# Optimization experiments

Hardware: AMD Instinct MI355X
Metric: run time of the kernel (lower is better)

## Reference

```python
import jax, jax.numpy as jnp
import numpy as np

# ---- production-scale dims ----
U, I, D = 51200, 25600, 64          # users, items, embed_size
E, EP = 1_000_000, 100_000          # train edges, pos/neg scoring edges
K = 8                               # topk similar users (FFT filter length)
NF = K // 2 + 1                     # rfft bins
CL_BS = 256                         # contrastive chunk size (U % CL_BS == 0)
TEMP = 0.2                          # args.temperature
N_LAYERS = 2                        # args.layers


def setup_inputs() -> dict:
    key = jax.random.key(0)
    ks = jax.random.split(key, 14)
    return {
        "user_emb": jax.random.normal(ks[0], (U, D), jnp.float32) * 0.1,
        "item_emb": jax.random.normal(ks[1], (I, D), jnp.float32) * 0.1,
        "W": jax.random.normal(ks[2], (D, D), jnp.float32) * (1.0 / np.sqrt(D)),
        "a": jax.random.normal(ks[3], (D,), jnp.float32) * 0.1,
        "WU": jax.random.normal(ks[4], (D, D), jnp.float32) * (1.0 / np.sqrt(D)),
        "aU": jax.random.normal(ks[5], (2 * D,), jnp.float32) * 0.1,
        "complex_weight": jax.random.normal(ks[6], (1, NF, D, 2), jnp.float32) * 0.02,
        "rate_src": jax.random.randint(ks[7], (E,), 0, U),
        "rate_dst": jax.random.randint(ks[8], (E,), 0, I),
        "pos_u": jax.random.randint(ks[9], (EP,), 0, U),
        "pos_i": jax.random.randint(ks[10], (EP,), 0, I),
        "neg_u": jax.random.randint(ks[11], (EP,), 0, U),
        "neg_i": jax.random.randint(ks[12], (EP,), 0, I),
        "nbr_idx": jax.random.randint(ks[13], (U, K), 0, U),
    }


def _propagate(src_feat, src_idx, dst_idx, n_dst):
    """DGRecLayer: degree-normalized mean aggregation over bipartite edges."""
    msg = src_feat[src_idx]                                       # [E, D] gather
    agg = jax.ops.segment_sum(msg, dst_idx, num_segments=n_dst)   # [n_dst, D] scatter
    deg = jax.ops.segment_sum(jnp.ones((src_idx.shape[0],), src_feat.dtype),
                              dst_idx, num_segments=n_dst)
    return agg / jnp.maximum(deg, 1.0)[:, None]


def _layer_attention(ls, W, a):
    t = jnp.stack(ls, axis=0)                                     # [L+1, N, D]
    alpha = jax.nn.softmax(jnp.einsum('lnd,de,e->ln', t, W, a), axis=0)
    return jnp.einsum('lnd,ln->nd', t, alpha)


def _anchor_user_embed(user_emb, WU, aU, complex_weight, nbr_idx):
    # Original detaches user embeddings to numpy for the FAISS path.
    ue = jax.lax.stop_gradient(user_emb)
    simu = ue[nbr_idx]                                            # [U, K, D]
    x = jnp.fft.rfft(simu, axis=1, norm='ortho')                  # [U, NF, D]
    wc = complex_weight[..., 0] + 1j * complex_weight[..., 1]     # [1, NF, D]
    simu = jnp.fft.irfft(x * wc, n=K, axis=1, norm='ortho')       # [U, K, D]
    Wsimu = jnp.einsum('ukd,de->uke', simu, WU)                   # [U, K, D]
    Wu = jnp.broadcast_to((ue @ WU)[:, None, :], Wsimu.shape)     # [U, K, D]
    e = jnp.concatenate([Wsimu, Wu], axis=2) @ aU                 # [U, K]
    e = jnp.where(e > 0, e, 0.1 * e)                              # LeakyReLU(0.1)
    alpha = jax.nn.softmax(e, axis=1)
    return jnp.einsum('uke,uk->ue', Wsimu, alpha)                 # [U, D]


def _chunk_contrast(r1, r2):
    B = r1.shape[0]
    n1 = jnp.linalg.norm(r1, axis=-1, keepdims=True)
    n2 = jnp.linalg.norm(r2, axis=-1, keepdims=True)
    s11 = (r1 @ r1.T) / (n1 @ n1.T + 1e-6) / TEMP
    c12 = (r1 @ r2.T) / (n1 @ n2.T + 1e-6) / TEMP
    s22 = (r2 @ r2.T) / (n2 @ n2.T + 1e-6) / TEMP
    c21 = (r2 @ r1.T) / (n2 @ n1.T + 1e-6) / TEMP
    mask = jax.nn.one_hot(jnp.arange(B), 2 * B, dtype=r1.dtype) * (-1e10)
    logits = jnp.concatenate(
        [jnp.concatenate([s11, c12], axis=-1) + mask,
         jnp.concatenate([s22, c21], axis=-1) + mask], axis=0)     # [2B, 2B]
    labels = jnp.concatenate([jnp.arange(B) + B, jnp.arange(B) + B])
    logz = jax.scipy.special.logsumexp(logits, axis=-1)
    return logz - logits[jnp.arange(2 * B), labels]                # per-example CE


def reference(user_emb, item_emb, W, a, WU, aU, complex_weight,
              rate_src, rate_dst, pos_u, pos_i, neg_u, neg_i, nbr_idx):
    h_u, h_i = user_emb, item_emb
    users, items = [h_u], [h_i]
    for _ in range(N_LAYERS):
        new_i = _propagate(h_u, rate_src, rate_dst, I)   # user -> item ('rate')
        new_u = _propagate(h_i, rate_dst, rate_src, U)   # item -> user ('rated by')
        h_u, h_i = new_u, new_i
        users.append(h_u)
        items.append(h_i)
    hu = _layer_attention(users, W, a)                   # [U, D]
    hi = _layer_attention(items, W, a)                   # [I, D]

    anchor = _anchor_user_embed(user_emb, WU, aU, complex_weight, nbr_idx)
    r1 = hu.reshape(-1, CL_BS, D)
    r2 = anchor.reshape(-1, CL_BS, D)
    loss_contrast = jax.vmap(_chunk_contrast)(r1, r2).mean()

    score_pos = jnp.sum(hu[pos_u] * hi[pos_i], axis=-1, keepdims=True)  # u_dot_v
    score_neg = jnp.sum(hu[neg_u] * hi[neg_i], axis=-1, keepdims=True)
    return score_pos, score_neg, loss_contrast
```

## Files before the change

kernel.cpp:

```cpp
#include <hip/hip_runtime.h>
#include <hip/hip_bf16.h>

constexpr int U_  = 51200;
constexpr int I_  = 25600;
constexpr int E_  = 1000000;
constexpr int EP_ = 100000;
constexpr int CB_ = 256;
constexpr int NCHUNK_ = U_ / CB_;
constexpr size_t UD_ = (size_t)U_ * 64;
constexpr size_t ID_ = (size_t)I_ * 64;
constexpr int NBK_ = 200;
constexpr int CAP_ = 8192;
constexpr int TILE_ = 4096;
constexpr int NBA_ = (E_ + TILE_ - 1) / TILE_;
constexpr int NANC_ = U_ / 16;
constexpr int NCVT_ = (int)((UD_ + ID_) / (8 * 256));

constexpr float SCALE_E_  = 16.f;
constexpr float ISCALE_E_ = 1.f / 16.f;
constexpr float SCALE_1_  = 64.f;
constexpr float ISCALE_1_ = 1.f / 64.f;

constexpr size_t OFF_LOSS  = 0;
constexpr size_t OFF_FLAG  = 1;
constexpr size_t OFF_CURU  = 8;
constexpr size_t OFF_CURI  = 208;
constexpr size_t MEMSET_BYTES = 408 * 4;
constexpr size_t OFF_VEC   = 448;
constexpr size_t OFF_BBU   = 640;
constexpr size_t OFF_BBI   = 848;
constexpr size_t OFF_ROWU  = 1088;
constexpr size_t OFF_ROWI  = ((OFF_ROWU + U_ + 1 + 63) / 64) * 64;
constexpr size_t OFF_CSRU  = ((OFF_ROWI + I_ + 1 + 63) / 64) * 64;
constexpr size_t OFF_CSRI  = OFF_CSRU + E_;
constexpr size_t OFF_U1    = ((OFF_CSRI + E_ + 63) / 64) * 64;
constexpr size_t OFF_I1    = OFF_U1 + UD_;
constexpr size_t OFF_HU    = OFF_I1 + ID_;
constexpr size_t OFF_HI    = OFF_HU + UD_;
constexpr size_t OFF_ANC   = OFF_HI + ID_;
constexpr size_t OFF_UE8   = OFF_ANC + UD_;
constexpr size_t OFF_IE8   = OFF_UE8 + UD_ / 4;
constexpr size_t OFF_U18   = OFF_IE8 + ID_ / 4;
constexpr size_t OFF_I18   = OFF_U18 + UD_ / 4;

#define DEVI static __device__ __forceinline__

typedef _Float16 h2v __attribute__((ext_vector_type(2)));
typedef _Float16 f16x8 __attribute__((ext_vector_type(8)));
typedef float floatx4 __attribute__((ext_vector_type(4)));
typedef unsigned short u16x8 __attribute__((ext_vector_type(8)));

DEVI float b2f(__hip_bfloat16 x) { return __bfloat162float(x); }

DEVI float bfb2f(unsigned short b) {
  unsigned u = ((unsigned)b) << 16; float f; __builtin_memcpy(&f, &u, 4); return f;
}

DEVI float ldf(const void* p, size_t i, int isf32) {
  if (isf32) return ((const float*)p)[i];
  return b2f(((const __hip_bfloat16*)p)[i]);
}

DEVI float frcp(float x) { return __builtin_amdgcn_rcpf(x); }

DEVI float fexp2(float x) {
#if __has_builtin(__builtin_amdgcn_exp2f)
  return __builtin_amdgcn_exp2f(x);
#else
  return exp2f(x);
#endif
}

DEVI float fp8_dec(unsigned v) {
#if __has_builtin(__builtin_amdgcn_cvt_f32_fp8)
  return __builtin_amdgcn_cvt_f32_fp8(v, 0);
#else
  unsigned b = v & 0xFF;
  if (!(b & 0x78)) return 0.f;
  unsigned short h = (unsigned short)(((b & 0x80) << 8) | (((b & 0x7f) + (8 << 3)) << 7));
  _Float16 hf; __builtin_memcpy(&hf, &h, 2);
  return (float)hf;
#endif
}

#if __has_builtin(__builtin_amdgcn_cvt_f32_fp8)
#define FP8D(w, s) __builtin_amdgcn_cvt_f32_fp8((w), (s))
#else
#define FP8D(w, s) fp8_dec(((w) >> (8 * (s))) & 0xFF)
#endif

DEVI unsigned fp8_enc_pk(float a, float b) {
#if __has_builtin(__builtin_amdgcn_cvt_pk_fp8_f32)
  return __builtin_amdgcn_cvt_pk_fp8_f32(a, b, 0u, false);
#else
  auto enc1 = [](float f) -> unsigned {
    _Float16 hf = (_Float16)f; unsigned short hb; __builtin_memcpy(&hb, &hf, 2);
    int s = hb >> 15, e = (hb >> 10) & 31, m = hb & 1023;
    int e8 = e - 15 + 7;
    int m3 = (m + ((1 << 6) + ((m >> 7) & 1))) >> 7;
    if (m3 > 7) { m3 = 0; e8++; }
    if (e8 <= 0) return (unsigned)(s << 7);
    if (e8 > 15) { e8 = 15; m3 = 6; }
    return (unsigned)((s << 7) | (e8 << 3) | m3);
  };
  return enc1(a) | (enc1(b) << 8);
#endif
}

DEVI int waveInclScan(int v, int lane) {
  #pragma unroll
  for (int off = 1; off < 64; off <<= 1) {
    int t = __shfl_up(v, off, 64);
    if (lane >= off) v += t;
  }
  return v;
}

__global__ void prep_kernel(const unsigned short* __restrict__ ueu,
                            const void* __restrict__ W, const void* __restrict__ a,
                            const void* __restrict__ WU, const void* __restrict__ aU,
                            float* __restrict__ vecs, float* __restrict__ flag) {
  int cnt = 0;
  for (int i = 0; i < 256; i++) {
    int e = (ueu[i] >> 7) & 0xFF;
    if (e >= 130) cnt++;
  }
  int isf32 = (cnt >= 8);
  if (threadIdx.x == 0) *flag = isf32 ? 1.0f : 0.0f;
  int d = threadIdx.x;
  float s = 0.f, t1 = 0.f, t2 = 0.f;
  for (int e = 0; e < 64; e++) {
    s += ldf(W, d * 64 + e, isf32) * ldf(a, e, isf32);
    float wue = ldf(WU, d * 64 + e, isf32);
    t1 += wue * ldf(aU, e, isf32);
    t2 += wue * ldf(aU, 64 + e, isf32);
  }
  vecs[d] = s;
  vecs[64 + d] = t1;
  vecs[128 + d] = t2;
}

struct BktSmem {
  int histU[NBK_], histI[NBK_];
  int loffU[NBK_ + 1], loffI[NBK_ + 1];
  int cbU[NBK_], cbI[NBK_];
  int lcU[NBK_], lcI[NBK_];
  int wsU[4], wsI[4];
  unsigned recsU[TILE_], recsI[TILE_];
};
constexpr int WS_ = 72;
struct AncSmem {
  _Float16 WUt[64 * WS_];
  _Float16 mixS[16 * WS_];
  float invSe[16];
  int nbrS[128];
};
constexpr size_t FSA_SMEM = sizeof(BktSmem) > sizeof(AncSmem) ? sizeof(BktSmem) : sizeof(AncSmem);

DEVI void bucketA_body(char* smemRaw, int blk,
    const int* __restrict__ rs, const int* __restrict__ rd,
    unsigned* __restrict__ bufU, unsigned* __restrict__ bufI,
    int* __restrict__ curU, int* __restrict__ curI) {
  BktSmem& S = *(BktSmem*)smemRaw;
  int tid = threadIdx.x;
  int base = blk * TILE_;
  for (int i = tid; i < NBK_; i += 256) { S.histU[i] = 0; S.histI[i] = 0; }
  __syncthreads();
  int ss[16], dd[16];
  #pragma unroll
  for (int t = 0; t < 16; t++) {
    int e = base + t * 256 + tid;
    bool v = e < E_;
    ss[t] = v ? rs[e] : -1;
    dd[t] = v ? rd[e] : 0;
    if (v) {
      atomicAdd(&S.histU[ss[t] >> 8], 1);
      atomicAdd(&S.histI[dd[t] >> 7], 1);
    }
  }
  __syncthreads();
  if (tid < NBK_) {
    int cU = S.histU[tid];
    S.cbU[tid] = tid * CAP_ + (cU ? atomicAdd(&curU[tid], cU) : 0);
    int cI = S.histI[tid];
    S.cbI[tid] = tid * CAP_ + (cI ? atomicAdd(&curI[tid], cI) : 0);
  }
  int lane = tid & 63, wv = tid >> 6;
  int cvU = (tid < NBK_) ? S.histU[tid] : 0;
  int cvI = (tid < NBK_) ? S.histI[tid] : 0;
  int inU = waveInclScan(cvU, lane);
  int inI = waveInclScan(cvI, lane);
  if (lane == 63) { S.wsU[wv] = inU; S.wsI[wv] = inI; }
  __syncthreads();
  int woU = 0, woI = 0;
  for (int w = 0; w < wv; w++) { woU += S.wsU[w]; woI += S.wsI[w]; }
  if (tid < NBK_) {
    S.loffU[tid] = woU + inU - cvU;
    S.loffI[tid] = woI + inI - cvI;
  }
  if (tid == NBK_ - 1) {
    S.loffU[NBK_] = woU + inU;
    S.loffI[NBK_] = woI + inI;
  }
  __syncthreads();
  if (tid < NBK_) { S.lcU[tid] = S.loffU[tid]; S.lcI[tid] = S.loffI[tid]; }
  __syncthreads();
  #pragma unroll
  for (int t = 0; t < 16; t++) {
    if (ss[t] >= 0) {
      int b = ss[t] >> 8;
      int p = atomicAdd(&S.lcU[b], 1);
      S.recsU[p] = ((unsigned)(ss[t] & 255) << 17) | (unsigned)dd[t];
      b = dd[t] >> 7;
      p = atomicAdd(&S.lcI[b], 1);
      S.recsI[p] = ((unsigned)(dd[t] & 127) << 17) | (unsigned)ss[t];
    }
  }
  __syncthreads();
  int totU = S.loffU[NBK_];
  for (int p = tid; p < totU; p += 256) {
    int lo = 0, hi = NBK_;
    while (hi - lo > 1) { int mid = (lo + hi) >> 1; if (S.loffU[mid] <= p) lo = mid; else hi = mid; }
    bufU[S.cbU[lo] + (p - S.loffU[lo])] = S.recsU[p];
  }
  int totI = S.loffI[NBK_];
  for (int p = tid; p < totI; p += 256) {
    int lo = 0, hi = NBK_;
    while (hi - lo > 1) { int mid = (lo + hi) >> 1; if (S.loffI[mid] <= p) lo = mid; else hi = mid; }
    bufI[S.cbI[lo] + (p - S.loffI[lo])] = S.recsI[p];
  }
}

DEVI void anchor_body(char* smemRaw, int blk,
    const void* __restrict__ ue, const void* __restrict__ WU,
    const void* __restrict__ cw, const float* __restrict__ vecs,
    const int* __restrict__ nbr, float* __restrict__ out, int isf32) {
  AncSmem& S = *(AncSmem*)smemRaw;
  int tid = threadIdx.x;
  int wv = tid >> 6, lane = tid & 63;
  int ublk = blk * 16;

  #pragma unroll
  for (int it = 0; it < 16; it++) {
    int k = it * 4 + wv;
    S.WUt[lane * WS_ + k] = (_Float16)ldf(WU, (size_t)k * 64 + lane, isf32);
  }
  if (tid < 128) S.nbrS[tid] = nbr[ublk * 8 + tid];
  __syncthreads();

  float cw0 = ldf(cw, (0 * 64 + lane) * 2, isf32);
  float w1r = ldf(cw, (1 * 64 + lane) * 2, isf32), w1i = ldf(cw, (1 * 64 + lane) * 2 + 1, isf32);
  float w2r = ldf(cw, (2 * 64 + lane) * 2, isf32), w2i = ldf(cw, (2 * 64 + lane) * 2 + 1, isf32);
  float w3r = ldf(cw, (3 * 64 + lane) * 2, isf32), w3i = ldf(cw, (3 * 64 + lane) * 2 + 1, isf32);
  float cw4 = ldf(cw, (4 * 64 + lane) * 2, isf32);
  float v1 = vecs[64 + lane], v2 = vecs[128 + lane];
  const float c1 = 0.70710678118654752440f;

  float xc[8], xn[8];
  #pragma unroll
  for (int k = 0; k < 8; k++)
    xc[k] = ldf(ue, (size_t)S.nbrS[wv * 32 + k] * 64 + lane, isf32);

  for (int u4 = 0; u4 < 4; u4++) {
    int uL = wv * 4 + u4;
    int u = ublk + uL;
    if (u4 < 3) {
      #pragma unroll
      for (int k = 0; k < 8; k++)
        xn[k] = ldf(ue, (size_t)S.nbrS[wv * 32 + (u4 + 1) * 8 + k] * 64 + lane, isf32);
    }
    float sA = xc[1] - xc[3] - xc[5] + xc[7];
    float sB = xc[1] + xc[3] - xc[5] - xc[7];
    float ev = (xc[0] + xc[4]) + (xc[2] + xc[6]);
    float od = (xc[1] + xc[5]) + (xc[3] + xc[7]);
    float d04 = xc[0] - xc[4], d26 = xc[2] - xc[6];
    float X0r = ev + od;
    float X1r = d04 + c1 * sA;
    float X1i = -d26 - c1 * sB;
    float X2r = (xc[0] + xc[4]) - (xc[2] + xc[6]);
    float X2i = -(xc[1] - xc[3] + xc[5] - xc[7]);
    float X3r = d04 - c1 * sA;
    float X3i = d26 - c1 * sB;
    float X4r = ev - od;
    float Zr0 = X0r * cw0;
    float Zr1 = X1r * w1r - X1i * w1i, Zi1 = X1r * w1i + X1i * w1r;
    float Zr2 = X2r * w2r - X2i * w2i, Zi2 = X2r * w2i + X2i * w2r;
    float Zr3 = X3r * w3r - X3i * w3i, Zi3 = X3r * w3i + X3i * w3r;
    float Zr4 = X4r * cw4;
    float eP = Zr0 + Zr4, eM = Zr0 - Zr4;
    float t1 = c1 * (Zr1 - Zr3), t2 = c1 * (Zi1 + Zi3);
    float y[8];
    y[0] = eP + 2.f * (Zr1 + Zr2 + Zr3);
    y[1] = eM + 2.f * (t1 - t2 - Zi2);
    y[2] = eP + 2.f * (-Zi1 - Zr2 + Zi3);
    y[3] = eM + 2.f * (-t1 - t2 + Zi2);
    y[4] = eP + 2.f * (-Zr1 + Zr2 - Zr3);
    y[5] = eM + 2.f * (-t1 + t2 - Zi2);
    y[6] = eP + 2.f * (Zi1 - Zr2 - Zi3);
    y[7] = eM + 2.f * (t1 + t2 + Zi2);
    #pragma unroll
    for (int k = 0; k < 8; k++) y[k] *= 0.125f;

    float ek[8];
    #pragma unroll
    for (int k = 0; k < 8; k++) ek[k] = y[k] * v1;
    float q = ldf(ue, (size_t)u * 64 + lane, isf32) * v2;
    #pragma unroll
    for (int off = 32; off; off >>= 1) {
      #pragma unroll
      for (int k = 0; k < 8; k++) ek[k] += __shfl_xor(ek[k], off, 64);
      q += __shfl_xor(q, off, 64);
    }
    float m = -1e30f;
    #pragma unroll
    for (int k = 0; k < 8; k++) {
      float v = ek[k] + q;
      v = v > 0.f ? v : 0.1f * v;
      ek[k] = v;
      m = fmaxf(m, v);
    }
    float se = 0.f, wexp[8];
    #pragma unroll
    for (int k = 0; k < 8; k++) { wexp[k] = __expf(ek[k] - m); se += wexp[k]; }
    float mix = 0.f;
    #pragma unroll
    for (int k = 0; k < 8; k++) mix += wexp[k] * y[k];
    S.mixS[uL * WS_ + lane] = (_Float16)mix;
    if (lane == 0) S.invSe[uL] = frcp(se);
    #pragma unroll
    for (int k = 0; k < 8; k++) xc[k] = xn[k];
  }
  __syncthreads();

  int n = lane & 15, qd = lane >> 4;
  f16x8 A0 = *(const f16x8*)&S.mixS[(lane & 15) * WS_ + qd * 8];
  f16x8 A1 = *(const f16x8*)&S.mixS[(lane & 15) * WS_ + 32 + qd * 8];
  f16x8 B0 = *(const f16x8*)&S.WUt[(wv * 16 + n) * WS_ + qd * 8];
  f16x8 B1 = *(const f16x8*)&S.WUt[(wv * 16 + n) * WS_ + 32 + qd * 8];
  const floatx4 zero = {0.f, 0.f, 0.f, 0.f};
  floatx4 acc = __builtin_amdgcn_mfma_f32_16x16x32_f16(A0, B0, zero, 0, 0, 0);
  acc = __builtin_amdgcn_mfma_f32_16x16x32_f16(A1, B1, acc, 0, 0, 0);
  #pragma unroll
  for (int r = 0; r < 4; r++) {
    int m = qd * 4 + r;
    out[(size_t)(ublk + m) * 64 + wv * 16 + n] = acc[r] * S.invSe[m];
  }
}

DEVI void convert_body(int blk, const void* __restrict__ ue, const void* __restrict__ ie,
                       unsigned char* __restrict__ ue8, unsigned char* __restrict__ ie8,
                       int isf32) {
  size_t t = (size_t)blk * 256 + threadIdx.x;
  const void* src; unsigned* dst; size_t o;
  if (t < UD_ / 8) { src = ue; dst = (unsigned*)ue8; o = t; }
  else             { src = ie; dst = (unsigned*)ie8; o = t - UD_ / 8; }
  float v[8];
  if (isf32) {
    float4 f0 = ((const float4*)src)[2 * o];
    float4 f1 = ((const float4*)src)[2 * o + 1];
    v[0] = f0.x; v[1] = f0.y; v[2] = f0.z; v[3] = f0.w;
    v[4] = f1.x; v[5] = f1.y; v[6] = f1.z; v[7] = f1.w;
  } else {
    u16x8 h = ((const u16x8*)src)[o];
    #pragma unroll
    for (int i = 0; i < 8; i++) v[i] = bfb2f(h[i]);
  }
  unsigned lo = fp8_enc_pk(v[0] * SCALE_E_, v[1] * SCALE_E_) |
                (fp8_enc_pk(v[2] * SCALE_E_, v[3] * SCALE_E_) << 16);
  unsigned hi = fp8_enc_pk(v[4] * SCALE_E_, v[5] * SCALE_E_) |
                (fp8_enc_pk(v[6] * SCALE_E_, v[7] * SCALE_E_) << 16);
  dst[2 * o]     = lo;
  dst[2 * o + 1] = hi;
}

__global__ __launch_bounds__(256) void fusedA_kernel(
    const int* __restrict__ rs, const int* __restrict__ rd,
    unsigned* __restrict__ bufU, unsigned* __restrict__ bufI,
    int* __restrict__ curU, int* __restrict__ curI,
    const void* __restrict__ ue, const void* __restrict__ ie,
    const void* __restrict__ WU, const void* __restrict__ cw,
    const float* __restrict__ vecs, const int* __restrict__ nbr,
    float* __restrict__ anc, unsigned char* __restrict__ ue8,
    unsigned char* __restrict__ ie8, const float* __restrict__ flag) {
  __shared__ __align__(16) char smem[FSA_SMEM];
  if (blockIdx.x < NBA_) {
    bucketA_body(smem, blockIdx.x, rs, rd, bufU, bufI, curU, curI);
  } else if (blockIdx.x < NBA_ + NANC_) {
    anchor_body(smem, blockIdx.x - NBA_, ue, WU, cw, vecs, nbr, anc, *flag > 0.5f);
  } else {
    convert_body(blockIdx.x - NBA_ - NANC_, ue, ie, ue8, ie8, *flag > 0.5f);
  }
}

__global__ void scanBuckets_kernel(const int* __restrict__ curU,
                                   const int* __restrict__ curI,
                                   int* __restrict__ bbU, int* __restrict__ bbI,
                                   int* __restrict__ rowU, int* __restrict__ rowI) {
  __shared__ int ws[8];
  int tid = threadIdx.x;
  int lane = tid & 63, wv = tid >> 6;
  int vU = (tid < NBK_) ? curU[tid] : 0;
  int vI = (tid < NBK_) ? curI[tid] : 0;
  int iU = waveInclScan(vU, lane);
  int iI = waveInclScan(vI, lane);
  if (lane == 63) { ws[wv] = iU; ws[4 + wv] = iI; }
  __syncthreads();
  int oU = 0, oI = 0;
  for (int w = 0; w < wv; w++) { oU += ws[w]; oI += ws[4 + w]; }
  if (tid < NBK_) { bbU[tid] = oU + iU - vU; bbI[tid] = oI + iI - vI; }
  if (tid == NBK_ - 1) { bbU[NBK_] = oU + iU; bbI[NBK_] = oI + iI; }
  if (tid == 0) { rowU[U_] = E_; rowI[I_] = E_; }
}

__global__ __launch_bounds__(256) void bucketB_kernel(
    const unsigned* __restrict__ bufU, const unsigned* __restrict__ bufI,
    const int* __restrict__ curU, const int* __restrict__ curI,
    const int* __restrict__ bbU, const int* __restrict__ bbI,
    int* __restrict__ rowU, int* __restrict__ rowI,
    int* __restrict__ csrU, int* __restrict__ csrI) {
  __shared__ int stage[CAP_];
  __shared__ int cntk[256], offk[256];
  __shared__ int wsum[4];
  int tid = threadIdx.x, b = blockIdx.x;
  int side = b >= NBK_;
  int bb = side ? b - NBK_ : b;
  const unsigned* src = (side ? bufI : bufU) + (size_t)bb * CAP_;
  int total = side ? curI[bb] : curU[bb];
  int gbase = side ? bbI[bb] : bbU[bb];
  int kpb   = side ? 128 : 256;
  int* rowptr = side ? rowI : rowU;
  int* csr    = side ? csrI : csrU;
  cntk[tid] = 0;
  __syncthreads();
  for (int r = tid; r < total; r += 256) atomicAdd(&cntk[src[r] >> 17], 1);
  __syncthreads();
  int lane = tid & 63, wv = tid >> 6;
  int cv = (tid < kpb) ? cntk[tid] : 0;
  int incl = waveInclScan(cv, lane);
  if (lane == 63) wsum[wv] = incl;
  __syncthreads();
  int wvoff = 0;
  for (int w = 0; w < wv; w++) wvoff += wsum[w];
  int excl = wvoff + incl - cv;
  if (tid < kpb) {
    offk[tid] = excl;
    rowptr[bb * kpb + tid] = gbase + excl;
  }
  __syncthreads();
  for (int r = tid; r < total; r += 256) {
    unsigned rec = src[r];
    int slot = atomicAdd(&offk[rec >> 17], 1);
    if (slot < CAP_) stage[slot] = (int)(rec & 0x1FFFFu);
  }
  __syncthreads();
  for (int s = tid; s < total; s += 256) csr[gbase + s] = stage[s];
}

__global__ __launch_bounds__(256) void agg1_kernel(
    const unsigned char* __restrict__ ue8, const unsigned char* __restrict__ ie8,
    const int* __restrict__ rowU, const int* __restrict__ rowI,
    const int* __restrict__ csrU, const int* __restrict__ csrI,
    __hip_bfloat16* __restrict__ u1, __hip_bfloat16* __restrict__ i1,
    unsigned char* __restrict__ u18, unsigned char* __restrict__ i18) {
  int wv = threadIdx.x >> 6, lane = threadIdx.x & 63;
  int sub = lane >> 4, c16 = lane & 15;
  int side = blockIdx.x >= I_ / 4;
  int blk = side ? blockIdx.x - I_ / 4 : blockIdx.x;
  int r = blk * 4 + wv;
  const int* row = side ? rowU : rowI;
  const int* csr = side ? csrU : csrI;
  const unsigned char* src = side ? ie8 : ue8;
  __hip_bfloat16* out = side ? u1 : i1;
  unsigned char* out8 = side ? u18 : i18;
  int s0 = row[r], s1 = row[r + 1];
  float a4[4] = {0.f, 0.f, 0.f, 0.f};
  int j = s0;
  for (; j + 8 <= s1; j += 8) {
    int e0 = csr[j + sub], e1 = csr[j + 4 + sub];
    unsigned w0 = *(const unsigned*)(src + (size_t)e0 * 64 + c16 * 4);
    unsigned w1 = *(const unsigned*)(src + (size_t)e1 * 64 + c16 * 4);
    a4[0] += FP8D(w0, 0) + FP8D(w1, 0);
    a4[1] += FP8D(w0, 1) + FP8D(w1, 1);
    a4[2] += FP8D(w0, 2) + FP8D(w1, 2);
    a4[3] += FP8D(w0, 3) + FP8D(w1, 3);
  }
  if (j + 4 <= s1) {
    int e0 = csr[j + sub];
    unsigned w0 = *(const unsigned*)(src + (size_t)e0 * 64 + c16 * 4);
    a4[0] += FP8D(w0, 0); a4[1] += FP8D(w0, 1);
    a4[2] += FP8D(w0, 2); a4[3] += FP8D(w0, 3);
    j += 4;
  }
  int rem = s1 - j;
  if (sub < rem) {
    int e0 = csr[j + sub];
    unsigned w0 = *(const unsigned*)(src + (size_t)e0 * 64 + c16 * 4);
    a4[0] += FP8D(w0, 0); a4[1] += FP8D(w0, 1);
    a4[2] += FP8D(w0, 2); a4[3] += FP8D(w0, 3);
  }
  #pragma unroll
  for (int c = 0; c < 4; c++) {
    a4[c] += __shfl_xor(a4[c], 16, 64);
    a4[c] += __shfl_xor(a4[c], 32, 64);
  }
  float acc = sub == 0 ? a4[0] : sub == 1 ? a4[1] : sub == 2 ? a4[2] : a4[3];
  int col = c16 * 4 + sub;
  float val = acc * ISCALE_E_ * frcp(fmaxf((float)(s1 - s0), 1.0f));
  size_t idx = (size_t)r * 64 + col;
  out[idx] = __float2bfloat16(val);
  unsigned p = fp8_enc_pk(val * SCALE_1_, val * SCALE_1_);
  out8[idx] = (unsigned char)(p & 0xFF);
}

__global__ __launch_bounds__(256) void agg2attn_kernel(
    const unsigned char* __restrict__ u18, const unsigned char* __restrict__ i18,
    const __hip_bfloat16* __restrict__ u1, const __hip_bfloat16* __restrict__ i1,
    const void* __restrict__ ue, const void* __restrict__ ie,
    const int* __restrict__ rowU, const int* __restrict__ rowI,
    const int* __restrict__ csrU, const int* __restrict__ csrI,
    const float* __restrict__ vecs, float* __restrict__ hu, float* __restrict__ hi,
    const float* __restrict__ flag) {
  int isf32 = *flag > 0.5f;
  int wv = threadIdx.x >> 6, lane = threadIdx.x & 63;
  int sub = lane >> 4, c16 = lane & 15;
  int side = blockIdx.x >= I_ / 4;
  int blk = side ? blockIdx.x - I_ / 4 : blockIdx.x;
  int r = blk * 4 + wv;
  const int* row = side ? rowU : rowI;
  const int* csr = side ? csrU : csrI;
  const unsigned char* opp8 = side ? i18 : u18;
  const __hip_bfloat16* own1 = side ? u1 : i1;
  const void* base = side ? ue : ie;
  float* h = side ? hu : hi;
  int s0 = row[r], s1 = row[r + 1];
  float a4[4] = {0.f, 0.f, 0.f, 0.f};
  int j = s0;
  for (; j + 8 <= s1; j += 8) {
    int e0 = csr[j + sub], e1 = csr[j + 4 + sub];
    unsigned w0 = *(const unsigned*)(opp8 + (size_t)e0 * 64 + c16 * 4);
    unsigned w1 = *(const unsigned*)(opp8 + (size_t)e1 * 64 + c16 * 4);
    a4[0] += FP8D(w0, 0) + FP8D(w1, 0);
    a4[1] += FP8D(w0, 1) + FP8D(w1, 1);
    a4[2] += FP8D(w0, 2) + FP8D(w1, 2);
    a4[3] += FP8D(w0, 3) + FP8D(w1, 3);
  }
  if (j + 4 <= s1) {
    int e0 = csr[j + sub];
    unsigned w0 = *(const unsigned*)(opp8 + (size_t)e0 * 64 + c16 * 4);
    a4[0] += FP8D(w0, 0); a4[1] += FP8D(w0, 1);
    a4[2] += FP8D(w0, 2); a4[3] += FP8D(w0, 3);
    j += 4;
  }
  int rem = s1 - j;
  if (sub < rem) {
    int e0 = csr[j + sub];
    unsigned w0 = *(const unsigned*)(opp8 + (size_t)e0 * 64 + c16 * 4);
    a4[0] += FP8D(w0, 0); a4[1] += FP8D(w0, 1);
    a4[2] += FP8D(w0, 2); a4[3] += FP8D(w0, 3);
  }
  #pragma unroll
  for (int c = 0; c < 4; c++) {
    a4[c] += __shfl_xor(a4[c], 16, 64);
    a4[c] += __shfl_xor(a4[c], 32, 64);
  }
  float acc = sub == 0 ? a4[0] : sub == 1 ? a4[1] : sub == 2 ? a4[2] : a4[3];
  int col = c16 * 4 + sub;
  size_t idx = (size_t)r * 64 + col;
  float t2 = acc * ISCALE_1_ * frcp(fmaxf((float)(s1 - s0), 1.0f));
  float t0 = ldf(base, idx, isf32);
  float t1 = b2f(own1[idx]);
  float w = vecs[col];
  float p0 = t0 * w, p1 = t1 * w, p2 = t2 * w;
  #pragma unroll
  for (int off = 32; off; off >>= 1) {
    p0 += __shfl_xor(p0, off, 64);
    p1 += __shfl_xor(p1, off, 64);
    p2 += __shfl_xor(p2, off, 64);
  }
  float m = fmaxf(p0, fmaxf(p1, p2));
  float e0 = __expf(p0 - m), e1 = __expf(p1 - m), e2 = __expf(p2 - m);
  float inv = 1.0f / (e0 + e1 + e2);
  h[idx] = (t0 * e0 + t1 * e1 + t2 * e2) * inv;
}

constexpr int XS_ = 72;
constexpr float SC_  = 2.6857914f;
constexpr float EPS_ = 1e-6f;
constexpr float LN2_ = 0.6931471805599453f;
__global__ __launch_bounds__(1024) void contrast_kernel(
    const float* __restrict__ hu, const float* __restrict__ an,
    float* __restrict__ loss_acc) {
  __shared__ __align__(16) _Float16 Xh[512 * XS_];
  __shared__ float iN[512];
  int tid = threadIdx.x;
  int c = blockIdx.x;

  if (tid < 512) {
    int row = tid & 255;
    const float* r1 = (tid < 256 ? hu : an) + ((size_t)c * CB_ + row) * 64;
    float4 a4[16];
    float s1 = 0.f;
    #pragma unroll
    for (int t = 0; t < 16; t++) {
      a4[t] = ((const float4*)r1)[t];
      s1 += a4[t].x * a4[t].x + a4[t].y * a4[t].y + a4[t].z * a4[t].z + a4[t].w * a4[t].w;
    }
    float inv = frcp(sqrtf(s1));
    iN[tid] = inv;
    float sc = inv * SC_;
    #pragma unroll
    for (int t = 0; t < 8; t++) {
      f16x8 v;
      v[0] = (_Float16)(a4[2*t].x * sc);   v[1] = (_Float16)(a4[2*t].y * sc);
      v[2] = (_Float16)(a4[2*t].z * sc);   v[3] = (_Float16)(a4[2*t].w * sc);
      v[4] = (_Float16)(a4[2*t+1].x * sc); v[5] = (_Float16)(a4[2*t+1].y * sc);
      v[6] = (_Float16)(a4[2*t+1].z * sc); v[7] = (_Float16)(a4[2*t+1].w * sc);
      *(f16x8*)&Xh[tid * XS_ + t * 8] = v;
    }
  }
  __syncthreads();

  int l = tid & 63, wv = tid >> 6;
  int n = l & 15, q = l >> 4;
  int rb = wv * 32;
  f16x8 A[2][2];
  #pragma unroll
  for (int t = 0; t < 2; t++) {
    A[t][0] = *(const f16x8*)&Xh[(rb + t * 16 + n) * XS_ + q * 8];
    A[t][1] = *(const f16x8*)&Xh[(rb + t * 16 + n) * XS_ + 32 + q * 8];
  }
  float eNiR[2][4];
  #pragma unroll
  for (int t = 0; t < 2; t++)
    #pragma unroll
    for (int r = 0; r < 4; r++)
      eNiR[t][r] = EPS_ * iN[rb + t * 16 + q * 4 + r];
  float sums[2][4] = {{0,0,0,0},{0,0,0,0}};
  float labs2[2] = {0, 0};
  int selfn = q * 4;
  const floatx4 zero = {0.f, 0.f, 0.f, 0.f};
  for (int ct = 0; ct < 32; ct++) {
    f16x8 B0 = *(const f16x8*)&Xh[(ct * 16 + n) * XS_ + q * 8];
    f16x8 B1 = *(const f16x8*)&Xh[(ct * 16 + n) * XS_ + 32 + q * 8];
    float iNj = iN[ct * 16 + n];
    #pragma unroll
    for (int t = 0; t < 2; t++) {
      floatx4 acc = __builtin_amdgcn_mfma_f32_16x16x32_f16(A[t][0], B0, zero, 0, 0, 0);
      acc = __builtin_amdgcn_mfma_f32_16x16x32_f16(A[t][1], B1, acc, 0, 0, 0);
      int rtg = wv * 2 + t;
      if (ct == (rtg ^ 16)) {
        #pragma unroll
        for (int r = 0; r < 4; r++) {
          float G = acc[r];
          float u = eNiR[t][r] * iNj;
          float s2 = __builtin_fmaf(G, -u, G);
          sums[t][r] += fexp2(s2);
          if (n == selfn + r) labs2[t] += s2;
        }
      } else if (ct == rtg) {
        #pragma unroll
        for (int r = 0; r < 4; r++) {
          float G = acc[r];
          float u = eNiR[t][r] * iNj;
          float s2 = __builtin_fmaf(G, -u, G);
          float e = (n == selfn + r) ? 0.f : fexp2(s2);
          sums[t][r] += e;
        }
      } else {
        #pragma unroll
        for (int r = 0; r < 4; r++) {
          float G = acc[r];
          float u = eNiR[t][r] * iNj;
          float s2 = __builtin_fmaf(G, -u, G);
          sums[t][r] += fexp2(s2);
        }
      }
    }
  }
  #pragma unroll
  for (int off = 1; off <= 8; off <<= 1) {
    #pragma unroll
    for (int t = 0; t < 2; t++) {
      #pragma unroll
      for (int r = 0; r < 4; r++) sums[t][r] += __shfl_xor(sums[t][r], off, 64);
      labs2[t] += __shfl_xor(labs2[t], off, 64);
    }
  }
  float part = 0.f;
  if (n == 0) {
    #pragma unroll
    for (int t = 0; t < 2; t++) {
      float lt = 0.f;
      #pragma unroll
      for (int r = 0; r < 4; r++) lt += __logf(sums[t][r]);
      part += lt - labs2[t] * LN2_;
    }
  }
  #pragma unroll
  for (int off = 1; off < 64; off <<= 1) part += __shfl_xor(part, off, 64);
  if (l == 0) atomicAdd(loss_acc, part);
}

__global__ __launch_bounds__(256) void score_kernel(
    const float* __restrict__ hu, const float* __restrict__ hi,
    const int* __restrict__ pu, const int* __restrict__ pi,
    const int* __restrict__ nu, const int* __restrict__ ni,
    void* __restrict__ out, const float* __restrict__ flag) {
  int isf32 = *flag > 0.5f;
  int w = (blockIdx.x * 256 + threadIdx.x) >> 6;
  int lane = threadIdx.x & 63;
  int uu, ii;
  if (w < EP_) { uu = pu[w]; ii = pi[w]; }
  else         { uu = nu[w - EP_]; ii = ni[w - EP_]; }
  float p = hu[(size_t)uu * 64 + lane] * hi[(size_t)ii * 64 + lane];
  #pragma unroll
  for (int off = 32; off; off >>= 1) p += __shfl_xor(p, off, 64);
  if (lane == 0) {
    if (isf32) ((float*)out)[w] = p;
    else       ((__hip_bfloat16*)out)[w] = __float2bfloat16(p);
  }
}

__global__ void finalize_kernel(const float* __restrict__ loss_acc,
                                void* __restrict__ out,
                                const float* __restrict__ flag) {
  float v = loss_acc[0] * (1.0f / (float)(2 * CB_ * NCHUNK_));
  if (*flag > 0.5f) ((float*)out)[2 * EP_] = v;
  else              ((__hip_bfloat16*)out)[2 * EP_] = __float2bfloat16(v);
}

extern "C" void kernel_launch(void* const* d_in, const int* in_sizes, int n_in,
                              void* d_out, int out_size, void* d_ws, size_t ws_size,
                              hipStream_t stream) {
  const void* ue  = d_in[0];
  const void* ie  = d_in[1];
  const void* W   = d_in[2];
  const void* a   = d_in[3];
  const void* WU  = d_in[4];
  const void* aU  = d_in[5];
  const void* cw  = d_in[6];
  const int* rs  = (const int*)d_in[7];
  const int* rd  = (const int*)d_in[8];
  const int* pu  = (const int*)d_in[9];
  const int* pi  = (const int*)d_in[10];
  const int* nu  = (const int*)d_in[11];
  const int* ni  = (const int*)d_in[12];
  const int* nbr = (const int*)d_in[13];

  float* wsf  = (float*)d_ws;
  int*   wsi  = (int*)d_ws;
  float* loss = wsf + OFF_LOSS;
  float* flag = wsf + OFF_FLAG;
  int* curU   = wsi + OFF_CURU;
  int* curI   = wsi + OFF_CURI;
  float* vecs = wsf + OFF_VEC;
  int* bbU    = wsi + OFF_BBU;
  int* bbI    = wsi + OFF_BBI;
  int* rowU   = wsi + OFF_ROWU;
  int* rowI   = wsi + OFF_ROWI;
  int* csrU   = wsi + OFF_CSRU;
  int* csrI   = wsi + OFF_CSRI;
  __hip_bfloat16* u1 = (__hip_bfloat16*)(wsf + OFF_U1);
  __hip_bfloat16* i1 = (__hip_bfloat16*)(wsf + OFF_I1);
  float* hu   = wsf + OFF_HU;
  float* hi   = wsf + OFF_HI;
  float* anc  = wsf + OFF_ANC;
  unsigned char* ue8 = (unsigned char*)(wsf + OFF_UE8);
  unsigned char* ie8 = (unsigned char*)(wsf + OFF_IE8);
  unsigned char* u18 = (unsigned char*)(wsf + OFF_U18);
  unsigned char* i18 = (unsigned char*)(wsf + OFF_I18);
  unsigned* bufU = (unsigned*)(wsf + OFF_HU);
  unsigned* bufI = (unsigned*)(wsf + OFF_HI);

  hipMemsetAsync(d_ws, 0, MEMSET_BYTES, stream);
  prep_kernel<<<1, 64, 0, stream>>>((const unsigned short*)ue, W, a, WU, aU, vecs, flag);

  fusedA_kernel<<<NBA_ + NANC_ + NCVT_, 256, 0, stream>>>(
      rs, rd, bufU, bufI, curU, curI, ue, ie, WU, cw, vecs, nbr, anc, ue8, ie8, flag);
  scanBuckets_kernel<<<1, 256, 0, stream>>>(curU, curI, bbU, bbI, rowU, rowI);
  bucketB_kernel<<<2 * NBK_, 256, 0, stream>>>(bufU, bufI, curU, curI, bbU, bbI,
                                               rowU, rowI, csrU, csrI);

  agg1_kernel<<<(I_ + U_) / 4, 256, 0, stream>>>(ue8, ie8, rowU, rowI, csrU, csrI,
                                                 u1, i1, u18, i18);
  agg2attn_kernel<<<(I_ + U_) / 4, 256, 0, stream>>>(u18, i18, u1, i1, ue, ie,
                                                     rowU, rowI, csrU, csrI,
                                                     vecs, hu, hi, flag);

  contrast_kernel<<<NCHUNK_, 1024, 0, stream>>>(hu, anc, loss);

  score_kernel<<<(2 * EP_ * 64) / 256, 256, 0, stream>>>(hu, hi, pu, pi, nu, ni, d_out, flag);
  finalize_kernel<<<1, 1, 0, stream>>>(loss, d_out, flag);
}
```

Measured before the change: 367.6 us.

## Regroup kernel fusion to overlap anchor, convert and score work with aggregation stages

Splits the old fused bucket/anchor/convert launch and redistributes the pieces. The fp8 convert now runs alongside bucketB, and each half of the anchor computation is packed beside agg1 or agg2. The separate bucket-scan kernel is removed by having every bucketB block redo the 200-entry prefix scan itself. Contrast and score are merged into one 1024-thread launch. The aim is fewer launches and better filling of the GPU by pairing independent work with the dependent stages, at the cost of larger shared-memory footprints and mixed block types within each launch.

```diff
diff --git a/kernel.cpp b/kernel.cpp
--- a/kernel.cpp
+++ b/kernel.cpp
@@ -14,7 +14,10 @@
 constexpr int TILE_ = 4096;
 constexpr int NBA_ = (E_ + TILE_ - 1) / TILE_;
 constexpr int NANC_ = U_ / 16;
+constexpr int NANCH_ = NANC_ / 2;
 constexpr int NCVT_ = (int)((UD_ + ID_) / (8 * 256));
+constexpr int NAGG_ = (I_ + U_) / 4;
+constexpr int NSCB_ = (2 * EP_ * 64) / 1024;
 
 constexpr float SCALE_E_  = 16.f;
 constexpr float ISCALE_E_ = 1.f / 16.f;
@@ -27,8 +30,6 @@
 constexpr size_t OFF_CURI  = 208;
 constexpr size_t MEMSET_BYTES = 408 * 4;
 constexpr size_t OFF_VEC   = 448;
-constexpr size_t OFF_BBU   = 640;
-constexpr size_t OFF_BBI   = 848;
 constexpr size_t OFF_ROWU  = 1088;
 constexpr size_t OFF_ROWI  = ((OFF_ROWU + U_ + 1 + 63) / 64) * 64;
 constexpr size_t OFF_CSRU  = ((OFF_ROWI + I_ + 1 + 63) / 64) * 64;
@@ -148,22 +149,14 @@
   int wsU[4], wsI[4];
   unsigned recsU[TILE_], recsI[TILE_];
 };
-constexpr int WS_ = 72;
-struct AncSmem {
-  _Float16 WUt[64 * WS_];
-  _Float16 mixS[16 * WS_];
-  float invSe[16];
-  int nbrS[128];
-};
-constexpr size_t FSA_SMEM = sizeof(BktSmem) > sizeof(AncSmem) ? sizeof(BktSmem) : sizeof(AncSmem);
-
-DEVI void bucketA_body(char* smemRaw, int blk,
+
+__global__ __launch_bounds__(256) void bucketA_kernel(
     const int* __restrict__ rs, const int* __restrict__ rd,
     unsigned* __restrict__ bufU, unsigned* __restrict__ bufI,
     int* __restrict__ curU, int* __restrict__ curI) {
-  BktSmem& S = *(BktSmem*)smemRaw;
+  __shared__ __align__(16) BktSmem S;
   int tid = threadIdx.x;
-  int base = blk * TILE_;
+  int base = blockIdx.x * TILE_;
   for (int i = tid; i < NBK_; i += 256) { S.histU[i] = 0; S.histI[i] = 0; }
   __syncthreads();
   int ss[16], dd[16];
@@ -230,6 +223,14 @@
     bufI[S.cbI[lo] + (p - S.loffI[lo])] = S.recsI[p];
   }
 }
+
+constexpr int WS_ = 72;
+struct AncSmem {
+  _Float16 WUt[64 * WS_];
+  _Float16 mixS[16 * WS_];
+  float invSe[16];
+  int nbrS[128];
+};
 
 DEVI void anchor_body(char* smemRaw, int blk,
     const void* __restrict__ ue, const void* __restrict__ WU,
@@ -373,90 +374,82 @@
   dst[2 * o + 1] = hi;
 }
 
-__global__ __launch_bounds__(256) void fusedA_kernel(
-    const int* __restrict__ rs, const int* __restrict__ rd,
-    unsigned* __restrict__ bufU, unsigned* __restrict__ bufI,
-    int* __restrict__ curU, int* __restrict__ curI,
-    const void* __restrict__ ue, const void* __restrict__ ie,
-    const void* __restrict__ WU, const void* __restrict__ cw,
-    const float* __restrict__ vecs, const int* __restrict__ nbr,
-    float* __restrict__ anc, unsigned char* __restrict__ ue8,
-    unsigned char* __restrict__ ie8, const float* __restrict__ flag) {
-  __shared__ __align__(16) char smem[FSA_SMEM];
-  if (blockIdx.x < NBA_) {
-    bucketA_body(smem, blockIdx.x, rs, rd, bufU, bufI, curU, curI);
-  } else if (blockIdx.x < NBA_ + NANC_) {
-    anchor_body(smem, blockIdx.x - NBA_, ue, WU, cw, vecs, nbr, anc, *flag > 0.5f);
-  } else {
-    convert_body(blockIdx.x - NBA_ - NANC_, ue, ie, ue8, ie8, *flag > 0.5f);
-  }
-}
-
-__global__ void scanBuckets_kernel(const int* __restrict__ curU,
-                                   const int* __restrict__ curI,
-                                   int* __restrict__ bbU, int* __restrict__ bbI,
-                                   int* __restrict__ rowU, int* __restrict__ rowI) {
-  __shared__ int ws[8];
-  int tid = threadIdx.x;
-  int lane = tid & 63, wv = tid >> 6;
-  int vU = (tid < NBK_) ? curU[tid] : 0;
-  int vI = (tid < NBK_) ? curI[tid] : 0;
-  int iU = waveInclScan(vU, lane);
-  int iI = waveInclScan(vI, lane);
-  if (lane == 63) { ws[wv] = iU; ws[4 + wv] = iI; }
-  __syncthreads();
-  int oU = 0, oI = 0;
-  for (int w = 0; w < wv; w++) { oU += ws[w]; oI += ws[4 + w]; }
-  if (tid < NBK_) { bbU[tid] = oU + iU - vU; bbI[tid] = oI + iI - vI; }
-  if (tid == NBK_ - 1) { bbU[NBK_] = oU + iU; bbI[NBK_] = oI + iI; }
-  if (tid == 0) { rowU[U_] = E_; rowI[I_] = E_; }
-}
-
-__global__ __launch_bounds__(256) void bucketB_kernel(
+struct BktBSmem {
+  int stage[CAP_];
+  int cntk[256], offk[256];
+  int exclS[256];
+  int wsum[4], wsum2[4];
+};
+
+DEVI void bucketB_body(char* smemRaw, int b,
     const unsigned* __restrict__ bufU, const unsigned* __restrict__ bufI,
     const int* __restrict__ curU, const int* __restrict__ curI,
-    const int* __restrict__ bbU, const int* __restrict__ bbI,
     int* __restrict__ rowU, int* __restrict__ rowI,
     int* __restrict__ csrU, int* __restrict__ csrI) {
-  __shared__ int stage[CAP_];
-  __shared__ int cntk[256], offk[256];
-  __shared__ int wsum[4];
-  int tid = threadIdx.x, b = blockIdx.x;
+  BktBSmem& S = *(BktBSmem*)smemRaw;
+  int tid = threadIdx.x;
   int side = b >= NBK_;
   int bb = side ? b - NBK_ : b;
   const unsigned* src = (side ? bufI : bufU) + (size_t)bb * CAP_;
-  int total = side ? curI[bb] : curU[bb];
-  int gbase = side ? bbI[bb] : bbU[bb];
+  const int* cur = side ? curI : curU;
+  int total = cur[bb];
   int kpb   = side ? 128 : 256;
   int* rowptr = side ? rowI : rowU;
   int* csr    = side ? csrI : csrU;
-  cntk[tid] = 0;
-  __syncthreads();
-  for (int r = tid; r < total; r += 256) atomicAdd(&cntk[src[r] >> 17], 1);
-  __syncthreads();
+  if (b == 0 && tid == 0) { rowU[U_] = E_; rowI[I_] = E_; }
   int lane = tid & 63, wv = tid >> 6;
-  int cv = (tid < kpb) ? cntk[tid] : 0;
+  {
+    int v = (tid < NBK_) ? cur[tid] : 0;
+    int incl = waveInclScan(v, lane);
+    if (lane == 63) S.wsum2[wv] = incl;
+    S.cntk[tid] = 0;
+    __syncthreads();
+    int off = 0;
+    for (int w = 0; w < wv; w++) off += S.wsum2[w];
+    if (tid < NBK_) S.exclS[tid] = off + incl - v;
+    __syncthreads();
+  }
+  int gbase = S.exclS[bb];
+  for (int r = tid; r < total; r += 256) atomicAdd(&S.cntk[src[r] >> 17], 1);
+  __syncthreads();
+  int cv = (tid < kpb) ? S.cntk[tid] : 0;
   int incl = waveInclScan(cv, lane);
-  if (lane == 63) wsum[wv] = incl;
+  if (lane == 63) S.wsum[wv] = incl;
   __syncthreads();
   int wvoff = 0;
-  for (int w = 0; w < wv; w++) wvoff += wsum[w];
+  for (int w = 0; w < wv; w++) wvoff += S.wsum[w];
   int excl = wvoff + incl - cv;
   if (tid < kpb) {
-    offk[tid] = excl;
+    S.offk[tid] = excl;
     rowptr[bb * kpb + tid] = gbase + excl;
   }
   __syncthreads();
   for (int r = tid; r < total; r += 256) {
     unsigned rec = src[r];
-    int slot = atomicAdd(&offk[rec >> 17], 1);
-    if (slot < CAP_) stage[slot] = (int)(rec & 0x1FFFFu);
-  }
-  __syncthreads();
-  for (int s = tid; s < total; s += 256) csr[gbase + s] = stage[s];
-}
-
-__global__ __launch_bounds__(256) void agg1_kernel(
+    int slot = atomicAdd(&S.offk[rec >> 17], 1);
+    if (slot < CAP_) S.stage[slot] = (int)(rec & 0x1FFFFu);
+  }
+  __syncthreads();
+  for (int s = tid; s < total; s += 256) csr[gbase + s] = S.stage[s];
+}
+
+__global__ __launch_bounds__(256) void fusedB_kernel(
+    const unsigned* __restrict__ bufU, const unsigned* __restrict__ bufI,
+    const int* __restrict__ curU, const int* __restrict__ curI,
+    int* __restrict__ rowU, int* __restrict__ rowI,
+    int* __restrict__ csrU, int* __restrict__ csrI,
+    const void* __restrict__ ue, const void* __restrict__ ie,
+    unsigned char* __restrict__ ue8, unsigned char* __restrict__ ie8,
+    const float* __restrict__ flag) {
+  __shared__ __align__(16) char smem[sizeof(BktBSmem)];
+  if (blockIdx.x < 2 * NBK_) {
+    bucketB_body(smem, blockIdx.x, bufU, bufI, curU, curI, rowU, rowI, csrU, csrI);
+  } else {
+    convert_body(blockIdx.x - 2 * NBK_, ue, ie, ue8, ie8, *flag > 0.5f);
+  }
+}
+
+DEVI void agg1_body(int bid,
     const unsigned char* __restrict__ ue8, const unsigned char* __restrict__ ie8,
     const int* __restrict__ rowU, const int* __restrict__ rowI,
     const int* __restrict__ csrU, const int* __restrict__ csrI,
@@ -464,8 +457,8 @@
     unsigned char* __restrict__ u18, unsigned char* __restrict__ i18) {
   int wv = threadIdx.x >> 6, lane = threadIdx.x & 63;
   int sub = lane >> 4, c16 = lane & 15;
-  int side = blockIdx.x >= I_ / 4;
-  int blk = side ? blockIdx.x - I_ / 4 : blockIdx.x;
+  int side = bid >= I_ / 4;
+  int blk = side ? bid - I_ / 4 : bid;
   int r = blk * 4 + wv;
   const int* row = side ? rowU : rowI;
   const int* csr = side ? csrU : csrI;
@@ -512,19 +505,18 @@
   out8[idx] = (unsigned char)(p & 0xFF);
 }
 
-__global__ __launch_bounds__(256) void agg2attn_kernel(
+DEVI void agg2_body(int bid,
     const unsigned char* __restrict__ u18, const unsigned char* __restrict__ i18,
     const __hip_bfloat16* __restrict__ u1, const __hip_bfloat16* __restrict__ i1,
     const void* __restrict__ ue, const void* __restrict__ ie,
     const int* __restrict__ rowU, const int* __restrict__ rowI,
     const int* __restrict__ csrU, const int* __restrict__ csrI,
     const float* __restrict__ vecs, float* __restrict__ hu, float* __restrict__ hi,
-    const float* __restrict__ flag) {
-  int isf32 = *flag > 0.5f;
+    int isf32) {
   int wv = threadIdx.x >> 6, lane = threadIdx.x & 63;
   int sub = lane >> 4, c16 = lane & 15;
-  int side = blockIdx.x >= I_ / 4;
-  int blk = side ? blockIdx.x - I_ / 4 : blockIdx.x;
+  int side = bid >= I_ / 4;
+  int blk = side ? bid - I_ / 4 : bid;
   int r = blk * 4 + wv;
   const int* row = side ? rowU : rowI;
   const int* csr = side ? csrU : csrI;
@@ -583,17 +575,60 @@
   h[idx] = (t0 * e0 + t1 * e1 + t2 * e2) * inv;
 }
 
+__global__ __launch_bounds__(256) void fusedC1_kernel(
+    const void* __restrict__ ue, const void* __restrict__ ie,
+    const void* __restrict__ WU, const void* __restrict__ cw,
+    const float* __restrict__ vecs, const int* __restrict__ nbr,
+    float* __restrict__ anc,
+    const unsigned char* __restrict__ ue8, const unsigned char* __restrict__ ie8,
+    const int* __restrict__ rowU, const int* __restrict__ rowI,
+    const int* __restrict__ csrU, const int* __restrict__ csrI,
+    __hip_bfloat16* __restrict__ u1, __hip_bfloat16* __restrict__ i1,
+    unsigned char* __restrict__ u18, unsigned char* __restrict__ i18,
+    const float* __restrict__ flag) {
+  __shared__ __align__(16) char smem[sizeof(AncSmem)];
+  if (blockIdx.x < NANCH_) {
+    anchor_body(smem, blockIdx.x, ue, WU, cw, vecs, nbr, anc, *flag > 0.5f);
+  } else {
+    agg1_body(blockIdx.x - NANCH_, ue8, ie8, rowU, rowI, csrU, csrI, u1, i1, u18, i18);
+  }
+}
+
+__global__ __launch_bounds__(256) void fusedC2_kernel(
+    const void* __restrict__ ue, const void* __restrict__ ie,
+    const void* __restrict__ WU, const void* __restrict__ cw,
+    const float* __restrict__ vecs, const int* __restrict__ nbr,
+    float* __restrict__ anc,
+    const unsigned char* __restrict__ u18, const unsigned char* __restrict__ i18,
+    const __hip_bfloat16* __restrict__ u1, const __hip_bfloat16* __restrict__ i1,
+    const int* __restrict__ rowU, const int* __restrict__ rowI,
+    const int* __restrict__ csrU, const int* __restrict__ csrI,
+    float* __restrict__ hu, float* __restrict__ hi,
+    const float* __restrict__ flag) {
+  __shared__ __align__(16) char smem[sizeof(AncSmem)];
+  int isf32 = *flag > 0.5f;
+  if (blockIdx.x < NANCH_) {
+    anchor_body(smem, NANCH_ + blockIdx.x, ue, WU, cw, vecs, nbr, anc, isf32);
+  } else {
+    agg2_body(blockIdx.x - NANCH_, u18, i18, u1, i1, ue, ie,
+              rowU, rowI, csrU, csrI, vecs, hu, hi, isf32);
+  }
+}
+
 constexpr int XS_ = 72;
 constexpr float SC_  = 2.6857914f;
 constexpr float EPS_ = 1e-6f;
 constexpr float LN2_ = 0.6931471805599453f;
-__global__ __launch_bounds__(1024) void contrast_kernel(
+struct CtrSmem {
+  _Float16 Xh[512 * XS_];
+  float iN[512];
+};
+
+DEVI void contrast_body(char* smemRaw, int c,
     const float* __restrict__ hu, const float* __restrict__ an,
     float* __restrict__ loss_acc) {
-  __shared__ __align__(16) _Float16 Xh[512 * XS_];
-  __shared__ float iN[512];
+  CtrSmem& S = *(CtrSmem*)smemRaw;
   int tid = threadIdx.x;
-  int c = blockIdx.x;
 
   if (tid < 512) {
     int row = tid & 255;
@@ -606,7 +641,7 @@
       s1 += a4[t].x * a4[t].x + a4[t].y * a4[t].y + a4[t].z * a4[t].z + a4[t].w * a4[t].w;
     }
     float inv = frcp(sqrtf(s1));
-    iN[tid] = inv;
+    S.iN[tid] = inv;
     float sc = inv * SC_;
     #pragma unroll
     for (int t = 0; t < 8; t++) {
@@ -615,7 +650,7 @@
       v[2] = (_Float16)(a4[2*t].z * sc);   v[3] = (_Float16)(a4[2*t].w * sc);
       v[4] = (_Float16)(a4[2*t+1].x * sc); v[5] = (_Float16)(a4[2*t+1].y * sc);
       v[6] = (_Float16)(a4[2*t+1].z * sc); v[7] = (_Float16)(a4[2*t+1].w * sc);
-      *(f16x8*)&Xh[tid * XS_ + t * 8] = v;
+      *(f16x8*)&S.Xh[tid * XS_ + t * 8] = v;
     }
   }
   __syncthreads();
@@ -626,23 +661,23 @@
   f16x8 A[2][2];
   #pragma unroll
   for (int t = 0; t < 2; t++) {
-    A[t][0] = *(const f16x8*)&Xh[(rb + t * 16 + n) * XS_ + q * 8];
-    A[t][1] = *(const f16x8*)&Xh[(rb + t * 16 + n) * XS_ + 32 + q * 8];
+    A[t][0] = *(const f16x8*)&S.Xh[(rb + t * 16 + n) * XS_ + q * 8];
+    A[t][1] = *(const f16x8*)&S.Xh[(rb + t * 16 + n) * XS_ + 32 + q * 8];
   }
   float eNiR[2][4];
   #pragma unroll
   for (int t = 0; t < 2; t++)
     #pragma unroll
     for (int r = 0; r < 4; r++)
-      eNiR[t][r] = EPS_ * iN[rb + t * 16 + q * 4 + r];
+      eNiR[t][r] = EPS_ * S.iN[rb + t * 16 + q * 4 + r];
   float sums[2][4] = {{0,0,0,0},{0,0,0,0}};
   float labs2[2] = {0, 0};
   int selfn = q * 4;
   const floatx4 zero = {0.f, 0.f, 0.f, 0.f};
   for (int ct = 0; ct < 32; ct++) {
-    f16x8 B0 = *(const f16x8*)&Xh[(ct * 16 + n) * XS_ + q * 8];
-    f16x8 B1 = *(const f16x8*)&Xh[(ct * 16 + n) * XS_ + 32 + q * 8];
-    float iNj = iN[ct * 16 + n];
+    f16x8 B0 = *(const f16x8*)&S.Xh[(ct * 16 + n) * XS_ + q * 8];
+    f16x8 B1 = *(const f16x8*)&S.Xh[(ct * 16 + n) * XS_ + 32 + q * 8];
+    float iNj = S.iN[ct * 16 + n];
     #pragma unroll
     for (int t = 0; t < 2; t++) {
       floatx4 acc = __builtin_amdgcn_mfma_f32_16x16x32_f16(A[t][0], B0, zero, 0, 0, 0);
@@ -701,13 +736,12 @@
   if (l == 0) atomicAdd(loss_acc, part);
 }
 
-__global__ __launch_bounds__(256) void score_kernel(
+DEVI void score_body(int blk,
     const float* __restrict__ hu, const float* __restrict__ hi,
     const int* __restrict__ pu, const int* __restrict__ pi,
     const int* __restrict__ nu, const int* __restrict__ ni,
-    void* __restrict__ out, const float* __restrict__ flag) {
-  int isf32 = *flag > 0.5f;
-  int w = (blockIdx.x * 256 + threadIdx.x) >> 6;
+    void* __restrict__ out, int isf32) {
+  int w = (blk * 1024 + threadIdx.x) >> 6;
   int lane = threadIdx.x & 63;
   int uu, ii;
   if (w < EP_) { uu = pu[w]; ii = pi[w]; }
@@ -718,6 +752,21 @@
   if (lane == 0) {
     if (isf32) ((float*)out)[w] = p;
     else       ((__hip_bfloat16*)out)[w] = __float2bfloat16(p);
+  }
+}
+
+__global__ __launch_bounds__(1024) void fusedD_kernel(
+    const float* __restrict__ hu, const float* __restrict__ hi,
+    const float* __restrict__ an,
+    const int* __restrict__ pu, const int* __restrict__ pi,
+    const int* __restrict__ nu, const int* __restrict__ ni,
+    void* __restrict__ out, float* __restrict__ loss_acc,
+    const float* __restrict__ flag) {
+  __shared__ __align__(16) char smem[sizeof(CtrSmem)];
+  if (blockIdx.x < NCHUNK_) {
+    contrast_body(smem, blockIdx.x, hu, an, loss_acc);
+  } else {
+    score_body(blockIdx.x - NCHUNK_, hu, hi, pu, pi, nu, ni, out, *flag > 0.5f);
   }
 }
 
@@ -754,8 +803,6 @@
   int* curU   = wsi + OFF_CURU;
   int* curI   = wsi + OFF_CURI;
   float* vecs = wsf + OFF_VEC;
-  int* bbU    = wsi + OFF_BBU;
-  int* bbI    = wsi + OFF_BBI;
   int* rowU   = wsi + OFF_ROWU;
   int* rowI   = wsi + OFF_ROWI;
   int* csrU   = wsi + OFF_CSRU;
@@ -775,20 +822,21 @@
   hipMemsetAsync(d_ws, 0, MEMSET_BYTES, stream);
   prep_kernel<<<1, 64, 0, stream>>>((const unsigned short*)ue, W, a, WU, aU, vecs, flag);
 
-  fusedA_kernel<<<NBA_ + NANC_ + NCVT_, 256, 0, stream>>>(
-      rs, rd, bufU, bufI, curU, curI, ue, ie, WU, cw, vecs, nbr, anc, ue8, ie8, flag);
-  scanBuckets_kernel<<<1, 256, 0, stream>>>(curU, curI, bbU, bbI, rowU, rowI);
-  bucketB_kernel<<<2 * NBK_, 256, 0, stream>>>(bufU, bufI, curU, curI, bbU, bbI,
-                                               rowU, rowI, csrU, csrI);
-
-  agg1_kernel<<<(I_ + U_) / 4, 256, 0, stream>>>(ue8, ie8, rowU, rowI, csrU, csrI,
-                                                 u1, i1, u18, i18);
-  agg2attn_kernel<<<(I_ + U_) / 4, 256, 0, stream>>>(u18, i18, u1, i1, ue, ie,
-                                                     rowU, rowI, csrU, csrI,
-                                                     vecs, hu, hi, flag);
-
-  contrast_kernel<<<NCHUNK_, 1024, 0, stream>>>(hu, anc, loss);
-
-  score_kernel<<<(2 * EP_ * 64) / 256, 256, 0, stream>>>(hu, hi, pu, pi, nu, ni, d_out, flag);
+  bucketA_kernel<<<NBA_, 256, 0, stream>>>(rs, rd, bufU, bufI, curU, curI);
+
+  fusedB_kernel<<<2 * NBK_ + NCVT_, 256, 0, stream>>>(
+      bufU, bufI, curU, curI, rowU, rowI, csrU, csrI, ue, ie, ue8, ie8, flag);
+
+  fusedC1_kernel<<<NANCH_ + NAGG_, 256, 0, stream>>>(
+      ue, ie, WU, cw, vecs, nbr, anc, ue8, ie8, rowU, rowI, csrU, csrI,
+      u1, i1, u18, i18, flag);
+
+  fusedC2_kernel<<<NANCH_ + NAGG_, 256, 0, stream>>>(
+      ue, ie, WU, cw, vecs, nbr, anc, u18, i18, u1, i1,
+      rowU, rowI, csrU, csrI, hu, hi, flag);
+
+  fusedD_kernel<<<NCHUNK_ + NSCB_, 1024, 0, stream>>>(
+      hu, hi, anc, pu, pi, nu, ni, d_out, loss, flag);
+
   finalize_kernel<<<1, 1, 0, stream>>>(loss, d_out, flag);
 }
```

After: 404.0 us. 1.1x slower.
